# Performance work log

Hardware: AMD Instinct MI355X
Metric: run time of the kernel (lower is better)

## Reference

```python
import jax, jax.numpy as jnp
import numpy as np

N = 8192
IN_F = 256
OUT_F = 128


def setup_inputs() -> dict:
    key = jax.random.key(0)
    k1, k2, k3, k4, k5, k6 = jax.random.split(key, 6)
    input = jax.random.normal(k1, (N, IN_F), dtype=jnp.float32)
    adj = jax.random.randint(k2, (N, N), 0, 2, dtype=jnp.int32)
    # xavier-uniform-like init scaled by gain=0.5
    def xavier(k, shape, gain=0.5):
        fan_in, fan_out = shape[0], shape[1]
        lim = gain * np.sqrt(6.0 / (fan_in + fan_out))
        return jax.random.uniform(k, shape, dtype=jnp.float32, minval=-lim, maxval=lim)
    W_s = xavier(k3, (IN_F, OUT_F))
    a_s = xavier(k4, (OUT_F, 1))
    W_n = xavier(k5, (IN_F, OUT_F))
    a_n = xavier(k6, (OUT_F, 1))
    return {"input": input, "adj": adj, "W_s": W_s, "a_s": a_s, "W_n": W_n, "a_n": a_n}


def reference(input, adj, W_s, a_s, W_n, a_n):
    # Projections: [N, out_features]
    h_s = input @ W_s
    h_n = input @ W_n
    # Additive attention logits: e[i, j] = relu((h_s @ a_s)[i] + (h_n @ a_n)[j])
    e = jax.nn.relu((h_s @ a_s) + (h_n @ a_n).T)  # [N, N]
    # Masked softmax over neighbors (dim=1)
    attention = jnp.where(adj > 0, e, jnp.float32(-9e15))
    attention = jax.nn.softmax(attention, axis=1)
    # Self-scaling term (sum of softmax rows, kept for faithfulness)
    attention_sum = jnp.sum(attention, axis=-1, keepdims=True)
    attention_s = 1.0 / (1.0 + attention_sum)
    # Dropout is identity in eval mode (p=0 / training=False)
    h_prime = attention_s * h_s + attention @ h_n
    # concat=True -> elu activation
    return jax.nn.elu(h_prime)
```

## Files before the change

### kernel.cpp

```cpp
#include <hip/hip_runtime.h>
#include <math.h>

#define NN 8192

typedef short short8 __attribute__((ext_vector_type(8)));
typedef float f32x4 __attribute__((ext_vector_type(4)));

__device__ __forceinline__ float eluf(float x) {
  return x > 0.f ? x : (__expf(x) - 1.f);
}
__device__ __forceinline__ unsigned short f2bf(float f) {
  union { float f; unsigned u; } v; v.f = f;
  unsigned r = v.u + 0x7fffu + ((v.u >> 16) & 1u);
  return (unsigned short)(r >> 16);
}
__device__ __forceinline__ unsigned pack4(int4 v, int sh) {
  return ((unsigned)(v.x & 1) << sh) | ((unsigned)(v.y & 1) << (sh + 1)) |
         ((unsigned)(v.z & 1) << (sh + 2)) | ((unsigned)(v.w & 1) << (sh + 3));
}

__global__ __launch_bounds__(256) void k_pre(const float* __restrict__ X,
                                             const int* __restrict__ A,
                                             const float* __restrict__ Ws,
                                             const float* __restrict__ Wn,
                                             const float* __restrict__ as_,
                                             const float* __restrict__ an_,
                                             float* __restrict__ Hs,
                                             unsigned short* __restrict__ HnT,
                                             float* __restrict__ es_out,
                                             float* __restrict__ en_out,
                                             unsigned* __restrict__ P) {
  __shared__ float4 lin4[8 * 64];
  const int bid = blockIdx.x;
  const int q5 = bid / 5, r5 = bid - q5 * 5;
  const int t = threadIdx.x;

  if (r5 == 4) {
    const int row0 = q5 * 32;
#pragma unroll 1
    for (int k = 0; k < 32; ++k) {
      int g = t + k * 256;
      int rr = g >> 8;
      int c8 = g & 255;
      const int4* src = (const int4*)(A + (size_t)(row0 + rr) * NN + c8 * 32);
      int4 v0 = src[0], v1 = src[1], v2 = src[2], v3 = src[3];
      int4 v4 = src[4], v5 = src[5], v6 = src[6], v7 = src[7];
      unsigned w = pack4(v0, 0)  | pack4(v1, 4)  | pack4(v2, 8)  | pack4(v3, 12) |
                   pack4(v4, 16) | pack4(v5, 20) | pack4(v6, 24) | pack4(v7, 28);
      P[(size_t)(row0 + rr) * 256 + c8] = w;
    }
    return;
  }

  const int i0 = (q5 * 4 + r5) * 8;
  const float4* Xg = (const float4*)X + (size_t)i0 * 64;
  lin4[t] = Xg[t];
  lin4[t + 256] = Xg[t + 256];
  __syncthreads();
  const int c = t & 127;
  const int rh = t >> 7;
  float accs[4], accn[4];
#pragma unroll
  for (int r = 0; r < 4; ++r) { accs[r] = 0.f; accn[r] = 0.f; }
  for (int k = 0; k < 256; k += 4) {
    float ws0 = Ws[(k + 0) * 128 + c], ws1 = Ws[(k + 1) * 128 + c];
    float ws2 = Ws[(k + 2) * 128 + c], ws3 = Ws[(k + 3) * 128 + c];
    float wn0 = Wn[(k + 0) * 128 + c], wn1 = Wn[(k + 1) * 128 + c];
    float wn2 = Wn[(k + 2) * 128 + c], wn3 = Wn[(k + 3) * 128 + c];
#pragma unroll
    for (int r = 0; r < 4; ++r) {
      float4 iv = lin4[(rh * 4 + r) * 64 + (k >> 2)];
      accs[r] = fmaf(iv.x, ws0, accs[r]); accs[r] = fmaf(iv.y, ws1, accs[r]);
      accs[r] = fmaf(iv.z, ws2, accs[r]); accs[r] = fmaf(iv.w, ws3, accs[r]);
      accn[r] = fmaf(iv.x, wn0, accn[r]); accn[r] = fmaf(iv.y, wn1, accn[r]);
      accn[r] = fmaf(iv.z, wn2, accn[r]); accn[r] = fmaf(iv.w, wn3, accn[r]);
    }
  }
#pragma unroll
  for (int r = 0; r < 4; ++r)
    Hs[(size_t)(i0 + rh * 4 + r) * 128 + c] = accs[r];
  {
    union { unsigned short us[4]; ushort4 u4; } pk;
#pragma unroll
    for (int r = 0; r < 4; ++r) pk.us[r] = f2bf(accn[r]);
    *(ushort4*)(HnT + (size_t)(i0 >> 3) * 1024 + c * 8 + rh * 4) = pk.u4;
  }
  float* red = (float*)lin4;
  const int wv = t >> 6, ln = t & 63;
  __syncthreads();
  {
    float av = as_[c];
#pragma unroll
    for (int r = 0; r < 4; ++r) red[(rh * 4 + r) * 128 + c] = accs[r] * av;
  }
  __syncthreads();
#pragma unroll
  for (int h = 0; h < 2; ++h) {
    int row = wv * 2 + h;
    float p = red[row * 128 + ln] + red[row * 128 + 64 + ln];
#pragma unroll
    for (int off = 32; off >= 1; off >>= 1) p += __shfl_down(p, off);
    if (ln == 0) es_out[i0 + row] = __expf(p);
  }
  __syncthreads();
  {
    float av = an_[c];
#pragma unroll
    for (int r = 0; r < 4; ++r) red[(rh * 4 + r) * 128 + c] = accn[r] * av;
  }
  __syncthreads();
#pragma unroll
  for (int h = 0; h < 2; ++h) {
    int row = wv * 2 + h;
    float p = red[row * 128 + ln] + red[row * 128 + 64 + ln];
#pragma unroll
    for (int off = 32; off >= 1; off >>= 1) p += __shfl_down(p, off);
    if (ln == 0) en_out[i0 + row] = __expf(p);
  }
}

__global__ __launch_bounds__(1024, 4) void k_main(const unsigned* __restrict__ Pk,
                                                  const unsigned short* __restrict__ HnT,
                                                  const float* __restrict__ es_g,
                                                  const float* __restrict__ en_g,
                                                  float* __restrict__ HsOut) {
  __shared__ __align__(16) char smem[65536];
  float* en_lds = (float*)smem;
  unsigned* bits_lds = (unsigned*)(smem + 32768);
  float* cmb = (float*)smem;
  __shared__ float zsh[8][32];
  __shared__ float zf[32];

  const int t = threadIdx.x;
  const int wv = t >> 6;
  const int fp = wv >> 3;
  const int jp = wv & 7;
  const int ln = t & 63;
  const int q = ln >> 4;
  const int m = ln & 15;
  const int row0 = blockIdx.x * 32;

  {
    float4* dst = (float4*)en_lds;
    const float4* s4 = (const float4*)en_g;
    dst[t] = s4[t];
    dst[t + 1024] = s4[t + 1024];
#pragma unroll
    for (int k = 0; k < 8; ++k) {
      int g = t + k * 1024;
      int rr = g >> 8;
      int c8 = g & 255;
      unsigned w = Pk[(size_t)(row0 + rr) * 256 + c8];
      bits_lds[(c8 >> 5) * 1024 + (c8 & 31) * 32 + rr] = w;
    }
  }

  const float sme0 = es_g[row0 + m];
  const float sme1 = es_g[row0 + 16 + m];
  const unsigned short* bptr = HnT + ((size_t)(jp * 128 + q) * 128 + fp * 64 + m) * 8;
  const float* nvl = en_lds + jp * 1024 + q * 8;
  const unsigned* bts = bits_lds + jp * 1024 + m;

  f32x4 acc0[4], acc1[4];
#pragma unroll
  for (int ftl = 0; ftl < 4; ++ftl) {
    acc0[ftl] = (f32x4){0.f, 0.f, 0.f, 0.f};
    acc1[ftl] = (f32x4){0.f, 0.f, 0.f, 0.f};
  }
  float zp0 = 0.f, zp1 = 0.f;

  union Breg { uint4 u; short8 s; };
  Breg breg[4];

  __syncthreads();

  breg[0].u = *(const uint4*)(bptr);
  breg[1].u = *(const uint4*)(bptr + 128);
  breg[2].u = *(const uint4*)(bptr + 256);
  breg[3].u = *(const uint4*)(bptr + 384);

#pragma unroll 2
  for (int tt = 0; tt < 32; ++tt) {
    short8 fr0, fr1;
    {
      float4 nv0 = *(const float4*)(nvl + tt * 32);
      float4 nv1 = *(const float4*)(nvl + tt * 32 + 4);
      const unsigned bw0 = bts[tt * 32];
      const unsigned bw1 = bts[tt * 32 + 16];
      const unsigned byte0 = (bw0 >> (q * 8)) & 0xffu;
      const unsigned byte1 = (bw1 >> (q * 8)) & 0xffu;
      float ev[8] = {nv0.x, nv0.y, nv0.z, nv0.w, nv1.x, nv1.y, nv1.z, nv1.w};
#pragma unroll
      for (int k = 0; k < 8; ++k) {
        float w0 = ((byte0 >> k) & 1u) ? fmaxf(sme0 * ev[k], 1.f) : 0.f;
        float w1 = ((byte1 >> k) & 1u) ? fmaxf(sme1 * ev[k], 1.f) : 0.f;
        zp0 += w0; zp1 += w1;
        fr0[k] = (short)f2bf(w0);
        fr1[k] = (short)f2bf(w1);
      }
    }
    __builtin_amdgcn_s_setprio(1);
    acc0[0] = __builtin_amdgcn_mfma_f32_16x16x32_bf16(fr0, breg[0].s, acc0[0], 0, 0, 0);
    acc1[0] = __builtin_amdgcn_mfma_f32_16x16x32_bf16(fr1, breg[0].s, acc1[0], 0, 0, 0);
    acc0[1] = __builtin_amdgcn_mfma_f32_16x16x32_bf16(fr0, breg[1].s, acc0[1], 0, 0, 0);
    acc1[1] = __builtin_amdgcn_mfma_f32_16x16x32_bf16(fr1, breg[1].s, acc1[1], 0, 0, 0);
    acc0[2] = __builtin_amdgcn_mfma_f32_16x16x32_bf16(fr0, breg[2].s, acc0[2], 0, 0, 0);
    acc1[2] = __builtin_amdgcn_mfma_f32_16x16x32_bf16(fr1, breg[2].s, acc1[2], 0, 0, 0);
    acc0[3] = __builtin_amdgcn_mfma_f32_16x16x32_bf16(fr0, breg[3].s, acc0[3], 0, 0, 0);
    acc1[3] = __builtin_amdgcn_mfma_f32_16x16x32_bf16(fr1, breg[3].s, acc1[3], 0, 0, 0);
    __builtin_amdgcn_s_setprio(0);
    {
      const unsigned short* p = bptr + (size_t)(tt + 1) * 4096;
      breg[0].u = *(const uint4*)(p);
      breg[1].u = *(const uint4*)(p + 128);
      breg[2].u = *(const uint4*)(p + 256);
      breg[3].u = *(const uint4*)(p + 384);
    }
  }

  {
    float zz0 = zp0, zz1 = zp1;
    zz0 += __shfl_down(zz0, 32); zz0 += __shfl_down(zz0, 16);
    zz1 += __shfl_down(zz1, 32); zz1 += __shfl_down(zz1, 16);
    if (fp == 0 && ln < 16) { zsh[jp][m] = zz0; zsh[jp][16 + m] = zz1; }
  }
  __syncthreads();

#define DUMP_SLOT(S)                                                        \
  {                                                                         \
    float* d = cmb + (S) * 2048 + q * 256 + m;                              \
    _Pragma("unroll") for (int ftl = 0; ftl < 4; ++ftl)                     \
      _Pragma("unroll") for (int reg = 0; reg < 4; ++reg) {                 \
        d[reg * 64 + ftl * 16] = acc0[ftl][reg];                            \
        d[1024 + reg * 64 + ftl * 16] = acc1[ftl][reg];                     \
      }                                                                     \
  }
#define ADD_SLOT(S)                                                         \
  {                                                                         \
    const float* d = cmb + (S) * 2048 + q * 256 + m;                        \
    _Pragma("unroll") for (int ftl = 0; ftl < 4; ++ftl)                     \
      _Pragma("unroll") for (int reg = 0; reg < 4; ++reg) {                 \
        acc0[ftl][reg] += d[reg * 64 + ftl * 16];                           \
        acc1[ftl][reg] += d[1024 + reg * 64 + ftl * 16];                    \
      }                                                                     \
  }
  if (jp >= 4) DUMP_SLOT(fp * 4 + (jp - 4));
  __syncthreads();
  if (jp < 4) ADD_SLOT(fp * 4 + jp);
  if (t < 32) {
    float z = zsh[0][t] + zsh[1][t] + zsh[2][t] + zsh[3][t] +
              zsh[4][t] + zsh[5][t] + zsh[6][t] + zsh[7][t];
    zf[t] = 1.f / z;
  }
  __syncthreads();
  if (jp == 2 || jp == 3) DUMP_SLOT(fp * 2 + (jp - 2));
  __syncthreads();
  if (jp < 2) ADD_SLOT(fp * 2 + jp);
  __syncthreads();
  if (jp == 1) DUMP_SLOT(fp);
  __syncthreads();
  if (jp == 0) { ADD_SLOT(fp); DUMP_SLOT(fp); }
  __syncthreads();
#undef DUMP_SLOT
#undef ADD_SLOT

  {
    const int row = t >> 5;
    const int f0 = (t & 31) * 4;
    const int fpx = f0 >> 6;
    f32x4 ssum = *(const f32x4*)&cmb[fpx * 2048 + row * 64 + (f0 & 63)];
    const float invz = zf[row];
    const size_t off = (size_t)(row0 + row) * 128 + f0;
    float4 h = *(const float4*)(HsOut + off);
    float4 o;
    o.x = eluf(fmaf(ssum[0], invz, 0.5f * h.x));
    o.y = eluf(fmaf(ssum[1], invz, 0.5f * h.y));
    o.z = eluf(fmaf(ssum[2], invz, 0.5f * h.z));
    o.w = eluf(fmaf(ssum[3], invz, 0.5f * h.w));
    *(float4*)(HsOut + off) = o;
  }
}

extern "C" void kernel_launch(void* const* d_in, const int* in_sizes, int n_in,
                              void* d_out, int out_size, void* d_ws, size_t ws_size,
                              hipStream_t stream) {
  const float* X   = (const float*)d_in[0];
  const int*   A   = (const int*)d_in[1];
  const float* Ws  = (const float*)d_in[2];
  const float* as_ = (const float*)d_in[3];
  const float* Wn  = (const float*)d_in[4];
  const float* an_ = (const float*)d_in[5];
  float* out = (float*)d_out;

  unsigned short* HnT = (unsigned short*)d_ws;
  float* es = (float*)(HnT + (size_t)128 * NN);
  float* en = es + NN;
  unsigned* P = (unsigned*)(en + NN);

  k_pre<<<1280, 256, 0, stream>>>(X, A, Ws, Wn, as_, an_, out, HnT, es, en, P);
  k_main<<<256, 1024, 0, stream>>>(P, HnT, es, en, out);
}
```

Measured before the change: 421.5 us.

## Fuse preprocessing and main attention kernel into one cooperative grid kernel

Replaces the two-kernel pipeline with a single cooperative kernel of 256 blocks. Each block packs its own 32 adjacency rows into a bitmask held in LDS, computes its projection slice, then waits on a grid-wide sync before running the MFMA aggregation. This avoids writing and re-reading the packed mask through global memory and removes one kernel launch. Even and odd blocks do the pack and projection phases in opposite order so memory-bound and compute-bound work overlap. The cost is a grid barrier and a dependence on cooperative launch, with the old two-kernel path kept as a fallback if that launch fails.

```diff
diff --git a/kernel.cpp b/kernel.cpp
--- a/kernel.cpp
+++ b/kernel.cpp
@@ -1,5 +1,8 @@
 #include <hip/hip_runtime.h>
+#include <hip/hip_cooperative_groups.h>
 #include <math.h>
+
+namespace cg = cooperative_groups;
 
 #define NN 8192
 
@@ -17,6 +20,260 @@
 __device__ __forceinline__ unsigned pack4(int4 v, int sh) {
   return ((unsigned)(v.x & 1) << sh) | ((unsigned)(v.y & 1) << (sh + 1)) |
          ((unsigned)(v.z & 1) << (sh + 2)) | ((unsigned)(v.w & 1) << (sh + 3));
+}
+
+__global__ __launch_bounds__(1024, 4) void k_fused(const float* __restrict__ X,
+                                                   const int* __restrict__ A,
+                                                   const float* __restrict__ Ws,
+                                                   const float* __restrict__ Wn,
+                                                   const float* __restrict__ as_,
+                                                   const float* __restrict__ an_,
+                                                   float* __restrict__ HsOut,
+                                                   unsigned short* __restrict__ HnT,
+                                                   float* __restrict__ es_g,
+                                                   float* __restrict__ en_g) {
+  __shared__ __align__(16) char smem[65536];
+  unsigned* bits_lds = (unsigned*)(smem + 32768);
+  __shared__ float zsh[8][32];
+  __shared__ float zf[32];
+
+  const int t = threadIdx.x;
+  const int bid = blockIdx.x;
+  const int row0 = bid * 32;
+
+  auto do_pack = [&]() {
+#pragma unroll 1
+    for (int k = 0; k < 8; ++k) {
+      int g = t + k * 1024;
+      int rr = g >> 8;
+      int c8 = g & 255;
+      const int4* src = (const int4*)(A + (size_t)(row0 + rr) * NN + c8 * 32);
+      int4 v0 = src[0], v1 = src[1], v2 = src[2], v3 = src[3];
+      int4 v4 = src[4], v5 = src[5], v6 = src[6], v7 = src[7];
+      unsigned w = pack4(v0, 0)  | pack4(v1, 4)  | pack4(v2, 8)  | pack4(v3, 12) |
+                   pack4(v4, 16) | pack4(v5, 20) | pack4(v6, 24) | pack4(v7, 28);
+      bits_lds[(c8 >> 5) * 1024 + (c8 & 31) * 32 + rr] = w;
+    }
+  };
+
+  auto do_proj = [&]() {
+    const int tl = t & 255;
+    const int u = t >> 8;
+    const int i0 = row0 + u * 8;
+    float4* S4 = (float4*)smem + u * 512;
+    const float4* Xg = (const float4*)X + (size_t)i0 * 64;
+    S4[tl] = Xg[tl];
+    S4[tl + 256] = Xg[tl + 256];
+    __syncthreads();
+    const int c = tl & 127;
+    const int rh = tl >> 7;
+    float accs[4], accn[4];
+#pragma unroll
+    for (int r = 0; r < 4; ++r) { accs[r] = 0.f; accn[r] = 0.f; }
+    for (int k = 0; k < 256; k += 4) {
+      float ws0 = Ws[(k + 0) * 128 + c], ws1 = Ws[(k + 1) * 128 + c];
+      float ws2 = Ws[(k + 2) * 128 + c], ws3 = Ws[(k + 3) * 128 + c];
+      float wn0 = Wn[(k + 0) * 128 + c], wn1 = Wn[(k + 1) * 128 + c];
+      float wn2 = Wn[(k + 2) * 128 + c], wn3 = Wn[(k + 3) * 128 + c];
+#pragma unroll
+      for (int r = 0; r < 4; ++r) {
+        float4 iv = S4[(rh * 4 + r) * 64 + (k >> 2)];
+        accs[r] = fmaf(iv.x, ws0, accs[r]); accs[r] = fmaf(iv.y, ws1, accs[r]);
+        accs[r] = fmaf(iv.z, ws2, accs[r]); accs[r] = fmaf(iv.w, ws3, accs[r]);
+        accn[r] = fmaf(iv.x, wn0, accn[r]); accn[r] = fmaf(iv.y, wn1, accn[r]);
+        accn[r] = fmaf(iv.z, wn2, accn[r]); accn[r] = fmaf(iv.w, wn3, accn[r]);
+      }
+    }
+#pragma unroll
+    for (int r = 0; r < 4; ++r)
+      HsOut[(size_t)(i0 + rh * 4 + r) * 128 + c] = accs[r];
+    {
+      union { unsigned short us[4]; ushort4 u4; } pk;
+#pragma unroll
+      for (int r = 0; r < 4; ++r) pk.us[r] = f2bf(accn[r]);
+      *(ushort4*)(HnT + (size_t)(i0 >> 3) * 1024 + c * 8 + rh * 4) = pk.u4;
+    }
+    float* red = (float*)S4;
+    const int wvl = tl >> 6, lnl = t & 63;
+    __syncthreads();
+    {
+      float av = as_[c];
+#pragma unroll
+      for (int r = 0; r < 4; ++r) red[(rh * 4 + r) * 128 + c] = accs[r] * av;
+    }
+    __syncthreads();
+#pragma unroll
+    for (int h = 0; h < 2; ++h) {
+      int row = wvl * 2 + h;
+      float p = red[row * 128 + lnl] + red[row * 128 + 64 + lnl];
+#pragma unroll
+      for (int off = 32; off >= 1; off >>= 1) p += __shfl_down(p, off);
+      if (lnl == 0) es_g[i0 + row] = __expf(p);
+    }
+    __syncthreads();
+    {
+      float av = an_[c];
+#pragma unroll
+      for (int r = 0; r < 4; ++r) red[(rh * 4 + r) * 128 + c] = accn[r] * av;
+    }
+    __syncthreads();
+#pragma unroll
+    for (int h = 0; h < 2; ++h) {
+      int row = wvl * 2 + h;
+      float p = red[row * 128 + lnl] + red[row * 128 + 64 + lnl];
+#pragma unroll
+      for (int off = 32; off >= 1; off >>= 1) p += __shfl_down(p, off);
+      if (lnl == 0) en_g[i0 + row] = __expf(p);
+    }
+  };
+
+  if ((bid & 1) == 0) { do_pack(); do_proj(); }
+  else                { do_proj(); do_pack(); }
+
+  __threadfence();
+  cg::this_grid().sync();
+
+  float* en_lds = (float*)smem;
+  float* cmb = (float*)smem;
+
+  const int wv = t >> 6;
+  const int fp = wv >> 3;
+  const int jp = wv & 7;
+  const int ln = t & 63;
+  const int q = ln >> 4;
+  const int m = ln & 15;
+
+  {
+    float4* dst = (float4*)en_lds;
+    const float4* s4 = (const float4*)en_g;
+    dst[t] = s4[t];
+    dst[t + 1024] = s4[t + 1024];
+  }
+
+  const float sme0 = es_g[row0 + m];
+  const float sme1 = es_g[row0 + 16 + m];
+  const unsigned short* bptr = HnT + ((size_t)(jp * 128 + q) * 128 + fp * 64 + m) * 8;
+  const float* nvl = en_lds + jp * 1024 + q * 8;
+  const unsigned* bts = bits_lds + jp * 1024 + m;
+
+  f32x4 acc0[4], acc1[4];
+#pragma unroll
+  for (int ftl = 0; ftl < 4; ++ftl) {
+    acc0[ftl] = (f32x4){0.f, 0.f, 0.f, 0.f};
+    acc1[ftl] = (f32x4){0.f, 0.f, 0.f, 0.f};
+  }
+  float zp0 = 0.f, zp1 = 0.f;
+
+  union Breg { uint4 u; short8 s; };
+  Breg breg[4];
+
+  __syncthreads();
+
+  breg[0].u = *(const uint4*)(bptr);
+  breg[1].u = *(const uint4*)(bptr + 128);
+  breg[2].u = *(const uint4*)(bptr + 256);
+  breg[3].u = *(const uint4*)(bptr + 384);
+
+#pragma unroll 2
+  for (int tt = 0; tt < 32; ++tt) {
+    short8 fr0, fr1;
+    {
+      float4 nv0 = *(const float4*)(nvl + tt * 32);
+      float4 nv1 = *(const float4*)(nvl + tt * 32 + 4);
+      const unsigned bw0 = bts[tt * 32];
+      const unsigned bw1 = bts[tt * 32 + 16];
+      const unsigned byte0 = (bw0 >> (q * 8)) & 0xffu;
+      const unsigned byte1 = (bw1 >> (q * 8)) & 0xffu;
+      float ev[8] = {nv0.x, nv0.y, nv0.z, nv0.w, nv1.x, nv1.y, nv1.z, nv1.w};
+#pragma unroll
+      for (int k = 0; k < 8; ++k) {
+        float w0 = ((byte0 >> k) & 1u) ? fmaxf(sme0 * ev[k], 1.f) : 0.f;
+        float w1 = ((byte1 >> k) & 1u) ? fmaxf(sme1 * ev[k], 1.f) : 0.f;
+        zp0 += w0; zp1 += w1;
+        fr0[k] = (short)f2bf(w0);
+        fr1[k] = (short)f2bf(w1);
+      }
+    }
+    __builtin_amdgcn_s_setprio(1);
+    acc0[0] = __builtin_amdgcn_mfma_f32_16x16x32_bf16(fr0, breg[0].s, acc0[0], 0, 0, 0);
+    acc1[0] = __builtin_amdgcn_mfma_f32_16x16x32_bf16(fr1, breg[0].s, acc1[0], 0, 0, 0);
+    acc0[1] = __builtin_amdgcn_mfma_f32_16x16x32_bf16(fr0, breg[1].s, acc0[1], 0, 0, 0);
+    acc1[1] = __builtin_amdgcn_mfma_f32_16x16x32_bf16(fr1, breg[1].s, acc1[1], 0, 0, 0);
+    acc0[2] = __builtin_amdgcn_mfma_f32_16x16x32_bf16(fr0, breg[2].s, acc0[2], 0, 0, 0);
+    acc1[2] = __builtin_amdgcn_mfma_f32_16x16x32_bf16(fr1, breg[2].s, acc1[2], 0, 0, 0);
+    acc0[3] = __builtin_amdgcn_mfma_f32_16x16x32_bf16(fr0, breg[3].s, acc0[3], 0, 0, 0);
+    acc1[3] = __builtin_amdgcn_mfma_f32_16x16x32_bf16(fr1, breg[3].s, acc1[3], 0, 0, 0);
+    __builtin_amdgcn_s_setprio(0);
+    {
+      const unsigned short* p = bptr + (size_t)(tt + 1) * 4096;
+      breg[0].u = *(const uint4*)(p);
+      breg[1].u = *(const uint4*)(p + 128);
+      breg[2].u = *(const uint4*)(p + 256);
+      breg[3].u = *(const uint4*)(p + 384);
+    }
+  }
+
+  {
+    float zz0 = zp0, zz1 = zp1;
+    zz0 += __shfl_down(zz0, 32); zz0 += __shfl_down(zz0, 16);
+    zz1 += __shfl_down(zz1, 32); zz1 += __shfl_down(zz1, 16);
+    if (fp == 0 && ln < 16) { zsh[jp][m] = zz0; zsh[jp][16 + m] = zz1; }
+  }
+  __syncthreads();
+
+#define DUMP_SLOT(S)                                                        \
+  {                                                                         \
+    float* d = cmb + (S) * 2048 + q * 256 + m;                              \
+    _Pragma("unroll") for (int ftl = 0; ftl < 4; ++ftl)                     \
+      _Pragma("unroll") for (int reg = 0; reg < 4; ++reg) {                 \
+        d[reg * 64 + ftl * 16] = acc0[ftl][reg];                            \
+        d[1024 + reg * 64 + ftl * 16] = acc1[ftl][reg];                     \
+      }                                                                     \
+  }
+#define ADD_SLOT(S)                                                         \
+  {                                                                         \
+    const float* d = cmb + (S) * 2048 + q * 256 + m;                        \
+    _Pragma("unroll") for (int ftl = 0; ftl < 4; ++ftl)                     \
+      _Pragma("unroll") for (int reg = 0; reg < 4; ++reg) {                 \
+        acc0[ftl][reg] += d[reg * 64 + ftl * 16];                           \
+        acc1[ftl][reg] += d[1024 + reg * 64 + ftl * 16];                    \
+      }                                                                     \
+  }
+  if (jp >= 4) DUMP_SLOT(fp * 4 + (jp - 4));
+  __syncthreads();
+  if (jp < 4) ADD_SLOT(fp * 4 + jp);
+  if (t < 32) {
+    float z = zsh[0][t] + zsh[1][t] + zsh[2][t] + zsh[3][t] +
+              zsh[4][t] + zsh[5][t] + zsh[6][t] + zsh[7][t];
+    zf[t] = 1.f / z;
+  }
+  __syncthreads();
+  if (jp == 2 || jp == 3) DUMP_SLOT(fp * 2 + (jp - 2));
+  __syncthreads();
+  if (jp < 2) ADD_SLOT(fp * 2 + jp);
+  __syncthreads();
+  if (jp == 1) DUMP_SLOT(fp);
+  __syncthreads();
+  if (jp == 0) { ADD_SLOT(fp); DUMP_SLOT(fp); }
+  __syncthreads();
+#undef DUMP_SLOT
+#undef ADD_SLOT
+
+  {
+    const int row = t >> 5;
+    const int f0 = (t & 31) * 4;
+    const int fpx = f0 >> 6;
+    f32x4 ssum = *(const f32x4*)&cmb[fpx * 2048 + row * 64 + (f0 & 63)];
+    const float invz = zf[row];
+    const size_t off = (size_t)(row0 + row) * 128 + f0;
+    float4 h = *(const float4*)(HsOut + off);
+    float4 o;
+    o.x = eluf(fmaf(ssum[0], invz, 0.5f * h.x));
+    o.y = eluf(fmaf(ssum[1], invz, 0.5f * h.y));
+    o.z = eluf(fmaf(ssum[2], invz, 0.5f * h.z));
+    o.w = eluf(fmaf(ssum[3], invz, 0.5f * h.w));
+    *(float4*)(HsOut + off) = o;
+  }
 }
 
 __global__ __launch_bounds__(256) void k_pre(const float* __restrict__ X,
@@ -297,6 +554,12 @@
   float* en = es + NN;
   unsigned* P = (unsigned*)(en + NN);
 
-  k_pre<<<1280, 256, 0, stream>>>(X, A, Ws, Wn, as_, an_, out, HnT, es, en, P);
-  k_main<<<256, 1024, 0, stream>>>(P, HnT, es, en, out);
-}
+  void* ka[] = {(void*)&X, (void*)&A, (void*)&Ws, (void*)&Wn, (void*)&as_,
+                (void*)&an_, (void*)&out, (void*)&HnT, (void*)&es, (void*)&en};
+  hipError_t err = hipLaunchCooperativeKernel((const void*)k_fused, dim3(256),
+                                              dim3(1024), ka, 0, stream);
+  if (err != hipSuccess) {
+    k_pre<<<1280, 256, 0, stream>>>(X, A, Ws, Wn, as_, an_, out, HnT, es, en, P);
+    k_main<<<256, 1024, 0, stream>>>(P, HnT, es, en, out);
+  }
+}
```

Result: slower. 629.5 us (+49.3%).
